# Kernel tuning notes

Hardware: AMD Instinct MI355X
Metric: run time of the kernel (lower is better)

Reference implementation:

```python
import jax, jax.numpy as jnp
import numpy as np

B, N, M, D, H = 2, 256, 64, 768, 12
HD = D // H  # head dim 64


def setup_inputs() -> dict:
    key = jax.random.key(0)
    ks = jax.random.split(key, 8)
    s = 0.02
    return {
        "x": jax.random.normal(ks[0], (B, N, D), jnp.float32),
        "sim_embeddings": jax.random.normal(ks[1], (B, N, M, D), jnp.float32),
        "Wq": jax.random.normal(ks[2], (D, D), jnp.float32) * s,
        "bq": jnp.zeros((D,), jnp.float32),
        "Wkv": jax.random.normal(ks[3], (D, 2 * D), jnp.float32) * s,
        "bkv": jnp.zeros((2 * D,), jnp.float32),
        "Wp": jax.random.normal(ks[4], (D, D), jnp.float32) * s,
        "bp": jnp.zeros((D,), jnp.float32),
    }


def reference(x, sim_embeddings, Wq, bq, Wkv, bkv, Wp, bp):
    # x: (B,N,D); sim_embeddings: (B,N,M,D)
    b, n, d = x.shape
    m = sim_embeddings.shape[2]
    scale = HD ** -0.5

    q = (x @ Wq + bq).reshape(b, n, H, HD).transpose(0, 2, 1, 3)  # (B,H,N,hd)

    kv_x = x @ Wkv + bkv                       # (B,N,2D)
    k_x, v_x = jnp.split(kv_x, 2, axis=-1)
    k_x = k_x.reshape(b, n, H, HD).transpose(0, 2, 1, 3)  # (B,H,N,hd) shared-global K
    v_x = v_x.reshape(b, n, H, HD).transpose(0, 2, 1, 3)

    kv_s = sim_embeddings @ Wkv + bkv          # (B,N,M,2D)
    k_s, v_s = jnp.split(kv_s, 2, axis=-1)
    k_s = k_s.reshape(b, n, m, H, HD).transpose(0, 3, 1, 2, 4)  # (B,H,N,M,hd) per-query local K
    v_s = v_s.reshape(b, n, m, H, HD).transpose(0, 3, 1, 2, 4)

    # scores over concatenated [global N keys | local M keys] without expanding K to (B,N,N+M,D)
    sg = jnp.einsum('bhnd,bhkd->bhnk', q, k_x) * scale   # (B,H,N,N)
    sl = jnp.einsum('bhnd,bhnmd->bhnm', q, k_s) * scale  # (B,H,N,M)
    attn = jax.nn.softmax(jnp.concatenate([sg, sl], axis=-1), axis=-1)
    ag, al = attn[..., :n], attn[..., n:]

    out = (jnp.einsum('bhnk,bhkd->bhnd', ag, v_x)
           + jnp.einsum('bhnm,bhnmd->bhnd', al, v_s))   # (B,H,N,hd)
    out = out.transpose(0, 2, 1, 3).reshape(b, n, d)
    return out @ Wp + bp
```

## Files before the change

### kernel.cpp

```cpp
#include <hip/hip_runtime.h>
#include <stdint.h>

#define DEV_INLINE __device__ __forceinline__

typedef __bf16 bf16x8 __attribute__((ext_vector_type(8)));
typedef float f32x4 __attribute__((ext_vector_type(4)));

typedef const __attribute__((address_space(1))) void* gas_ptr;
typedef __attribute__((address_space(3))) void* las_ptr;

DEV_INLINE unsigned short f2bf(float f) {
    union { __bf16 h; unsigned short u; } v;
    v.h = (__bf16)f;
    return v.u;
}

template <int N> DEV_INLINE void waitcnt_vm() {
    asm volatile("s_waitcnt vmcnt(%0)" :: "n"(N) : "memory");
}
DEV_INLINE void hard_barrier() {
    __builtin_amdgcn_sched_barrier(0);
    __builtin_amdgcn_s_barrier();
    __builtin_amdgcn_sched_barrier(0);
}

__global__ __launch_bounds__(256)
void prep_all_kernel(const float* __restrict__ x, unsigned short* __restrict__ xb,
                     const float* __restrict__ Wkv, unsigned short* __restrict__ wkvb,
                     const float* __restrict__ bq, const float* __restrict__ bkv,
                     float* __restrict__ bias1, float* __restrict__ zbuf,
                     const float* __restrict__ Wq, const float* __restrict__ Wp,
                     unsigned short* __restrict__ w1t, unsigned short* __restrict__ wpt,
                     const float* __restrict__ sim, unsigned short* __restrict__ simb) {
    __shared__ float tl[64][65];
    const int bid = blockIdx.x, t = threadIdx.x;
    if (bid >= 2124) {
        long i = (long)(bid - 2124) * 256 + t;
        const float4* sp = (const float4*)sim + i * 2;
        float4 a = sp[0], b = sp[1];
        union { bf16x8 v; unsigned short u[8]; } pk;
        pk.u[0] = f2bf(a.x); pk.u[1] = f2bf(a.y);
        pk.u[2] = f2bf(a.z); pk.u[3] = f2bf(a.w);
        pk.u[4] = f2bf(b.x); pk.u[5] = f2bf(b.y);
        pk.u[6] = f2bf(b.z); pk.u[7] = f2bf(b.w);
        ((bf16x8*)simb)[i] = pk.v;
        return;
    }
    if (bid < 1536) {
        const float* s; unsigned short* d; long i;
        if (bid < 384) { s = x;   d = xb;   i = (long)bid * 256 + t; }
        else           { s = Wkv; d = wkvb; i = (long)(bid - 384) * 256 + t; }
        float4 a = ((const float4*)s)[i];
        ushort4 o;
        o.x = f2bf(a.x); o.y = f2bf(a.y); o.z = f2bf(a.z); o.w = f2bf(a.w);
        ((ushort4*)d)[i] = o;
    } else if (bid < 1548) {
        int i = (bid - 1536) * 256 + t;
        if (i < 768) bias1[i] = bq[i];
        else if (i < 2304) bias1[i] = bkv[i - 768];
        else zbuf[i - 2304] = 0.f;
    } else {
        int tb = bid - 1548;
        int bx = tb % 48, by = tb / 48;
        const float* src; unsigned short* dst; int C;
        if (bx < 12)      { src = Wq;  dst = w1t;              C = 768; }
        else if (bx < 36) { src = Wkv; dst = w1t + 768L * 768; C = 1536; bx -= 12; }
        else              { src = Wp;  dst = wpt;              C = 768; bx -= 36; }
        int c0 = bx * 64, r0 = by * 64;
        int tx = t & 63, ty = t >> 6;
        #pragma unroll
        for (int i = 0; i < 64; i += 4)
            tl[ty + i][tx] = src[(long)(r0 + ty + i) * C + c0 + tx];
        __syncthreads();
        #pragma unroll
        for (int i = 0; i < 64; i += 4)
            dst[(long)(c0 + ty + i) * 768 + r0 + tx] = f2bf(tl[tx][ty + i]);
    }
}

template <int WM, int WN, int WAVES_M, bool G1E>
DEV_INLINE void gemm_body(const unsigned short* A, int lda,
                          const unsigned short* BT, int ldb,
                          const unsigned short* A2, int lda2,
                          const unsigned short* B2, int ldb2, int K1,
                          const float* bias, void* Cout, int ldc, int K,
                          const float* cin, int OUT, long obase, long tm, long tn,
                          unsigned short* As, unsigned short* Bs,
                          float* g1_qf, unsigned short* g1_qb,
                          unsigned short* g1_kxb, unsigned short* g1_vxT) {
    constexpr int TR = WAVES_M * WM * 16;
    constexpr int TC = (4 / WAVES_M) * WN * 16;
    constexpr int NL = TR / 32 + TC / 32;
    const int tid = threadIdx.x;
    const int w = tid >> 6, lane = tid & 63;
    const int lm = lane & 15, quad = lane >> 4;
    const int m_off = (w % WAVES_M) * WM * 16;
    const int n_off = (w / WAVES_M) * WN * 16;
    const int lrow8 = lane >> 3;
    const int lcol_sw = (((lane & 7) ^ lrow8) * 8);

    f32x4 acc[WM][WN];
    #pragma unroll
    for (int mi = 0; mi < WM; ++mi)
        #pragma unroll
        for (int ni = 0; ni < WN; ++ni) acc[mi][ni] = f32x4{0.f, 0.f, 0.f, 0.f};

    auto stage = [&](int k0, int pb) {
        const unsigned short* Ab; const unsigned short* Bb;
        int la, lb, kc;
        if (k0 < K1) { Ab = A;  Bb = BT; la = lda;  lb = ldb;  kc = k0; }
        else         { Ab = A2; Bb = B2; la = lda2; lb = ldb2; kc = k0 - K1; }
        unsigned short* Asb = As + pb * (TR * 64);
        unsigned short* Bsb = Bs + pb * (TC * 64);
        #pragma unroll
        for (int i = 0; i < TR / 32; ++i) {
            int rr = w * (TR / 4) + i * 8;
            const unsigned short* ga = Ab + (tm + rr + lrow8) * la + kc + lcol_sw;
            __builtin_amdgcn_global_load_lds((gas_ptr)ga, (las_ptr)(Asb + rr * 64), 16, 0, 0);
        }
        #pragma unroll
        for (int i = 0; i < TC / 32; ++i) {
            int rr = w * (TC / 4) + i * 8;
            const unsigned short* gb = Bb + (tn + rr + lrow8) * lb + kc + lcol_sw;
            __builtin_amdgcn_global_load_lds((gas_ptr)gb, (las_ptr)(Bsb + rr * 64), 16, 0, 0);
        }
    };

    stage(0, 0);
    const int nt = K >> 6;
    for (int t = 0; t < nt; ++t) {
        const int cur = t & 1;
        if (t + 1 < nt) {
            stage((t + 1) << 6, cur ^ 1);
            waitcnt_vm<NL>();
        } else {
            waitcnt_vm<0>();
        }
        hard_barrier();
        const unsigned short* Asb = As + cur * (TR * 64);
        const unsigned short* Bsb = Bs + cur * (TC * 64);
        #pragma unroll
        for (int kk = 0; kk < 2; ++kk) {
            bf16x8 af[WM], bfr[WN];
            #pragma unroll
            for (int mi = 0; mi < WM; ++mi) {
                int r = m_off + mi * 16 + lm;
                af[mi] = *(const bf16x8*)(Asb + r * 64 + (((kk * 4 + quad) ^ (r & 7)) * 8));
            }
            #pragma unroll
            for (int ni = 0; ni < WN; ++ni) {
                int r = n_off + ni * 16 + lm;
                bfr[ni] = *(const bf16x8*)(Bsb + r * 64 + (((kk * 4 + quad) ^ (r & 7)) * 8));
            }
            #pragma unroll
            for (int mi = 0; mi < WM; ++mi)
                #pragma unroll
                for (int ni = 0; ni < WN; ++ni)
                    acc[mi][ni] = __builtin_amdgcn_mfma_f32_16x16x32_bf16(
                        af[mi], bfr[ni], acc[mi][ni], 0, 0, 0);
        }
        hard_barrier();
    }

    #pragma unroll
    for (int mi = 0; mi < WM; ++mi) {
        #pragma unroll
        for (int ni = 0; ni < WN; ++ni) {
            long col = tn + n_off + ni * 16 + lm;
            float bv = bias[col];
            #pragma unroll
            for (int r = 0; r < 4; ++r) {
                long row = tm + m_off + mi * 16 + quad * 4 + r;
                float v = acc[mi][ni][r] + bv;
                if (G1E) {
                    if (col < 768) {
                        g1_qf[row * 768 + col] = v;
                        g1_qb[row * 768 + col] = f2bf(v);
                    } else if (col < 1536) {
                        g1_kxb[row * 768 + (col - 768)] = f2bf(v);
                    } else {
                        int j = (int)col - 1536, h = j >> 6, d = j & 63;
                        int bb = (int)row >> 8, nn = (int)row & 255;
                        g1_vxT[((long)(bb * 12 + h) * 64 + d) * 256 + nn] = f2bf(v);
                    }
                } else {
                    long idx = obase + row * ldc + col;
                    if (cin) v += cin[idx];
                    if (OUT == 0) ((float*)Cout)[idx] = v;
                    else ((unsigned short*)Cout)[idx] = f2bf(v);
                }
            }
        }
    }
}

template <int WM, int WN, int WAVES_M, bool G1E>
__global__ __launch_bounds__(256)
void gemm_bf16_kernel(const unsigned short* __restrict__ A, int lda,
                      const unsigned short* __restrict__ BT, int ldb,
                      const float* __restrict__ bias,
                      void* __restrict__ Cout, int ldc, int K,
                      const float* __restrict__ cin, int OUT,
                      long aZb, long aZh, long bZb, long bZh, long oZb, long oZh,
                      float* __restrict__ g1_qf, unsigned short* __restrict__ g1_qb,
                      unsigned short* __restrict__ g1_kxb,
                      unsigned short* __restrict__ g1_vxT) {
    constexpr int TR = WAVES_M * WM * 16;
    constexpr int TC = (4 / WAVES_M) * WN * 16;
    __shared__ unsigned short As[2 * TR * 64];
    __shared__ unsigned short Bs[2 * TC * 64];
    const int z = blockIdx.z, zb = z / 12, zh = z % 12;
    gemm_body<WM, WN, WAVES_M, G1E>(
        A + zb * aZb + zh * aZh, lda, BT + zb * bZb + zh * bZh, ldb,
        nullptr, 0, nullptr, 0, 1 << 30,
        bias, Cout, ldc, K, cin, OUT, zb * oZb + zh * oZh,
        (long)blockIdx.y * TR, (long)blockIdx.x * TC, As, Bs,
        g1_qf, g1_qb, g1_kxb, g1_vxT);
}

__global__ __launch_bounds__(256)
void gemm_qwsg_kernel(const unsigned short* __restrict__ qb,
                      const unsigned short* __restrict__ wkvb,
                      const unsigned short* __restrict__ kxb,
                      const float* __restrict__ zbuf,
                      unsigned short* __restrict__ qWb,
                      float* __restrict__ sgbuf) {
    __shared__ unsigned short As[2 * 64 * 64];
    __shared__ unsigned short Bs[2 * 64 * 64];
    int bid = blockIdx.x;
    if (bid < 1152) {
        int bx = bid % 12, by = (bid / 12) % 8, h = bid / 96;
        gemm_body<2, 2, 2, false>(
            qb + h * 64, 768, wkvb + h * 64, 1536,
            nullptr, 0, nullptr, 0, 1 << 30,
            zbuf, qWb, 768, 64, nullptr, 1, (long)h * 393216,
            (long)by * 64, (long)bx * 64, As, Bs,
            nullptr, nullptr, nullptr, nullptr);
    } else {
        int bid2 = bid - 1152;
        int bx = bid2 % 4, by = (bid2 / 4) % 4, z = bid2 / 16;
        int zb = z / 12, zh = z % 12;
        gemm_body<2, 2, 2, false>(
            qb + zb * 196608 + zh * 64, 768, kxb + zb * 196608 + zh * 64, 768,
            nullptr, 0, nullptr, 0, 1 << 30,
            zbuf, sgbuf, 256, 64, nullptr, 0,
            (long)zb * 786432 + (long)zh * 65536,
            (long)by * 64, (long)bx * 64, As, Bs,
            nullptr, nullptr, nullptr, nullptr);
    }
}

template <int WM, int WN, int WAVES_M>
__global__ __launch_bounds__(256)
void gemm_concat_kernel(const unsigned short* __restrict__ A, int lda, long aZb, long aZh,
                        const unsigned short* __restrict__ BT, int ldb, long bZb, long bZh,
                        const unsigned short* __restrict__ A2, int lda2, long a2Zb, long a2Zh,
                        const unsigned short* __restrict__ B2, int ldb2, long b2Zb, long b2Zh,
                        int K1, int K, const float* __restrict__ bias,
                        void* __restrict__ Cout, int ldc,
                        const float* __restrict__ cin, int OUT, long oZb, long oZh) {
    constexpr int TR = WAVES_M * WM * 16;
    constexpr int TC = (4 / WAVES_M) * WN * 16;
    __shared__ unsigned short As[2 * TR * 64];
    __shared__ unsigned short Bs[2 * TC * 64];
    const int z = blockIdx.z, zb = z / 12, zh = z % 12;
    gemm_body<WM, WN, WAVES_M, false>(
        A + zb * aZb + zh * aZh, lda, BT + zb * bZb + zh * bZh, ldb,
        A2 + zb * a2Zb + zh * a2Zh, lda2, B2 + zb * b2Zb + zh * b2Zh, ldb2, K1,
        bias, Cout, ldc, K, cin, OUT, zb * oZb + zh * oZh,
        (long)blockIdx.y * TR, (long)blockIdx.x * TC, As, Bs,
        nullptr, nullptr, nullptr, nullptr);
}

__global__ __launch_bounds__(256)
void slpart2_kernel(const unsigned short* __restrict__ simb,
                    const unsigned short* __restrict__ qWb,
                    float* __restrict__ sclp) {
    __shared__ unsigned short qw_s[16 * 784];
    __shared__ unsigned short ss[2][64 * 64];
    const int t = threadIdx.x;
    const int w = t >> 6, lane = t & 63;
    const int lm = lane & 15, quad = lane >> 4;
    const int lrow8 = lane >> 3;
    const int lcol_sw = ((lane & 7) ^ lrow8) * 8;
    const int n_ = blockIdx.x;
    const unsigned short* simn = simb + (long)n_ * 49152;

    auto stage = [&](int c, int pb) {
        unsigned short* dst = ss[pb];
        #pragma unroll
        for (int i = 0; i < 2; ++i) {
            int rr = w * 16 + i * 8;
            const unsigned short* ga = simn + (rr + lrow8) * 768 + c * 64 + lcol_sw;
            __builtin_amdgcn_global_load_lds((gas_ptr)ga, (las_ptr)(dst + rr * 64), 16, 0, 0);
        }
    };
    stage(0, 0);

    for (int idx = t; idx < 1152; idx += 256) {
        int h = idx / 96, c = idx - h * 96;
        *(bf16x8*)(qw_s + h * 784 + c * 8) =
            *(const bf16x8*)(qWb + ((long)h * 512 + n_) * 768 + c * 8);
    }
    __syncthreads();

    f32x4 acc = {};
    const int r = w * 16 + lm;
    for (int c = 0; c < 12; ++c) {
        const int cur = c & 1;
        if (c + 1 < 12) {
            stage(c + 1, cur ^ 1);
            waitcnt_vm<2>();
        } else {
            waitcnt_vm<0>();
        }
        hard_barrier();
        const unsigned short* buf = ss[cur];
        #pragma unroll
        for (int kk = 0; kk < 2; ++kk) {
            bf16x8 af = *(const bf16x8*)(buf + r * 64 + (((kk * 4 + quad) ^ (r & 7)) * 8));
            bf16x8 bfr = *(const bf16x8*)(qw_s + lm * 784 + c * 64 + kk * 32 + quad * 8);
            acc = __builtin_amdgcn_mfma_f32_16x16x32_bf16(af, bfr, acc, 0, 0, 0);
        }
        hard_barrier();
    }
    if (lm < 12) {
        float* dst = sclp + ((long)n_ * 12 + lm) * 64 + w * 16 + quad * 4;
        #pragma unroll
        for (int r2 = 0; r2 < 4; ++r2) dst[r2] = acc[r2];
    }
}

__global__ __launch_bounds__(256)
void attn2_kernel(const float* __restrict__ sim,
                  const float* __restrict__ qf,
                  const float* __restrict__ bkv,
                  const float* __restrict__ sclp,
                  const float* __restrict__ sgbuf,
                  unsigned short* __restrict__ agb,
                  float* __restrict__ outg0,
                  unsigned short* __restrict__ simbar) {
    __shared__ float slb_s[12];
    __shared__ float al_s[12][64];
    const int t = threadIdx.x;
    const int lane = t & 63, w = t >> 6;
    const int n_ = blockIdx.x, cg = blockIdx.y;
    const int b = n_ >> 8, n = n_ & 255;
    const float* simn = sim + (long)n_ * 49152;

    {
        float p0 = qf[(long)n_ * 768 + t] * bkv[t];
        float p1 = qf[(long)n_ * 768 + t + 256] * bkv[t + 256];
        float p2 = qf[(long)n_ * 768 + t + 512] * bkv[t + 512];
        #pragma unroll
        for (int off = 32; off > 0; off >>= 1) {
            p0 += __shfl_xor(p0, off);
            p1 += __shfl_xor(p1, off);
            p2 += __shfl_xor(p2, off);
        }
        if (lane == 0) { slb_s[w] = p0; slb_s[w + 4] = p1; slb_s[w + 8] = p2; }
    }
    __syncthreads();

    #pragma unroll
    for (int i = 0; i < 3; ++i) {
        const int h = w * 3 + i;
        const float* sgr = sgbuf + (long)(b * 12 + h) * 65536 + (long)n * 256;
        float v0 = sgr[lane] * 0.125f, v1 = sgr[lane + 64] * 0.125f,
              v2 = sgr[lane + 128] * 0.125f, v3 = sgr[lane + 192] * 0.125f;
        float v4 = (sclp[((long)n_ * 12 + h) * 64 + lane] + slb_s[h]) * 0.125f;
        float mx = fmaxf(fmaxf(fmaxf(v0, v1), fmaxf(v2, v3)), v4);
        #pragma unroll
        for (int off = 32; off > 0; off >>= 1) mx = fmaxf(mx, __shfl_xor(mx, off));
        float e0 = __expf(v0 - mx), e1 = __expf(v1 - mx), e2 = __expf(v2 - mx),
              e3 = __expf(v3 - mx), e4 = __expf(v4 - mx);
        float s = e0 + e1 + e2 + e3 + e4;
        #pragma unroll
        for (int off = 32; off > 0; off >>= 1) s += __shfl_xor(s, off);
        float inv = __frcp_rn(s);
        float al = e4 * inv;
        al_s[h][lane] = al;
        if (cg == 0) {
            unsigned short* agr = agb + (long)(b * 12 + h) * 65536 + (long)n * 256;
            agr[lane] = f2bf(e0 * inv); agr[lane + 64] = f2bf(e1 * inv);
            agr[lane + 128] = f2bf(e2 * inv); agr[lane + 192] = f2bf(e3 * inv);
            float am = al;
            #pragma unroll
            for (int off = 32; off > 0; off >>= 1) am += __shfl_xor(am, off);
            outg0[(long)n_ * 768 + h * 64 + lane] = am * bkv[768 + h * 64 + lane];
        }
    }
    __syncthreads();

    const int c = cg * 256 + t;
    float a[12];
    #pragma unroll
    for (int h = 0; h < 12; ++h) a[h] = 0.f;
    #pragma unroll 4
    for (int m = 0; m < 64; ++m) {
        float s = simn[(long)m * 768 + c];
        #pragma unroll
        for (int h = 0; h < 12; ++h) a[h] += al_s[h][m] * s;
    }
    #pragma unroll
    for (int h = 0; h < 12; ++h)
        simbar[((long)h * 512 + n_) * 768 + c] = f2bf(a[h]);
}


extern "C" void kernel_launch(void* const* d_in, const int* in_sizes, int n_in,
                              void* d_out, int out_size, void* d_ws, size_t ws_size,
                              hipStream_t stream) {
    const float* x   = (const float*)d_in[0];
    const float* sim = (const float*)d_in[1];
    const float* Wq  = (const float*)d_in[2];
    const float* bq  = (const float*)d_in[3];
    const float* Wkv = (const float*)d_in[4];
    const float* bkv = (const float*)d_in[5];
    const float* Wp  = (const float*)d_in[6];
    const float* bp  = (const float*)d_in[7];
    float* out = (float*)d_out;

    char* ws = (char*)d_ws;
    size_t off = 0;
    auto alloc = [&](size_t bytes) {
        char* p = ws + off;
        off += (bytes + 255) & ~(size_t)255;
        return p;
    };
    unsigned short* xb     = (unsigned short*)alloc(512UL * 768 * 2);
    unsigned short* w1t    = (unsigned short*)alloc(2304UL * 768 * 2);
    unsigned short* wkvb   = (unsigned short*)alloc(768UL * 1536 * 2);
    unsigned short* wpt    = (unsigned short*)alloc(768UL * 768 * 2);
    float*          qf     = (float*)alloc(512UL * 768 * 4);
    unsigned short* qb     = (unsigned short*)alloc(512UL * 768 * 2);
    unsigned short* kxb    = (unsigned short*)alloc(512UL * 768 * 2);
    unsigned short* vxT    = (unsigned short*)alloc(24UL * 64 * 256 * 2);
    unsigned short* qWb    = (unsigned short*)alloc(12UL * 512 * 768 * 2);
    unsigned short* simb   = (unsigned short*)alloc(512UL * 64 * 768 * 2);
    float*          sgbuf  = (float*)alloc(24UL * 65536 * 4);
    unsigned short* agb    = (unsigned short*)alloc(24UL * 65536 * 2);
    float*          outg0  = (float*)alloc(512UL * 768 * 4);
    float*          sclp   = (float*)alloc(512UL * 12 * 64 * 4);
    unsigned short* simbar = (unsigned short*)alloc(12UL * 512 * 768 * 2);
    unsigned short* attnb  = (unsigned short*)alloc(512UL * 768 * 2);
    float*          bias1  = (float*)alloc(2304UL * 4);
    float*          zbuf   = (float*)alloc(768UL * 4);

    prep_all_kernel<<<14412, 256, 0, stream>>>(
        x, xb, Wkv, wkvb, bq, bkv, bias1, zbuf, Wq, Wp, w1t, wpt, sim, simb);

    gemm_bf16_kernel<1, 2, 2, true><<<dim3(36, 16, 1), 256, 0, stream>>>(
        xb, 768, w1t, 768, bias1, nullptr, 768, 768, nullptr, 0,
        0, 0, 0, 0, 0, 0, qf, qb, kxb, vxT);

    gemm_qwsg_kernel<<<1536, 256, 0, stream>>>(qb, wkvb, kxb, zbuf, qWb, sgbuf);

    slpart2_kernel<<<512, 256, 0, stream>>>(simb, qWb, sclp);

    attn2_kernel<<<dim3(512, 3), 256, 0, stream>>>(
        sim, qf, bkv, sclp, sgbuf, agb, outg0, simbar);

    gemm_concat_kernel<1, 1, 2><<<dim3(2, 8, 24), 256, 0, stream>>>(
        simbar, 768, 196608, 393216,
        w1t + 1536L * 768, 768, 0, 49152,
        agb, 256, 786432, 65536,
        vxT, 256, 196608, 16384,
        768, 1024, zbuf, attnb, 768, outg0, 1, 196608, 64);

    gemm_bf16_kernel<1, 1, 2, false><<<dim3(24, 16, 1), 256, 0, stream>>>(
        attnb, 768, wpt, 768, bp, out, 768, 768, nullptr, 0,
        0, 0, 0, 0, 0, 0, nullptr, nullptr, nullptr, nullptr);
}
```

Baseline: 246.6 us.

## Fuse post-prep stages into one cooperative persistent kernel with grid syncs

Replaces the six kernel launches after prep with one cooperative kernel of 512 blocks that runs each stage in turn, separated by grid-wide syncs. The slpart and attn stages merge per row, so the local scores stay in LDS and the sclp buffer is gone. GEMM tile shapes change to a single 64x64 configuration, and the late GEMMs run on only 96 blocks. The aim is to remove launch gaps and a global round trip, at the cost of grid-sync overhead, less parallelism in the small GEMM phases, and each block doing three column groups serially in the attention phase.

New measurement: 706.1 us. 2.86x slower.

```diff
diff --git a/kernel.cpp b/kernel.cpp
--- a/kernel.cpp
+++ b/kernel.cpp
@@ -1,5 +1,8 @@
 #include <hip/hip_runtime.h>
+#include <hip/hip_cooperative_groups.h>
 #include <stdint.h>
+
+namespace cg = cooperative_groups;
 
 #define DEV_INLINE __device__ __forceinline__
 
@@ -194,217 +197,216 @@
     }
 }
 
-template <int WM, int WN, int WAVES_M, bool G1E>
-__global__ __launch_bounds__(256)
-void gemm_bf16_kernel(const unsigned short* __restrict__ A, int lda,
-                      const unsigned short* __restrict__ BT, int ldb,
-                      const float* __restrict__ bias,
-                      void* __restrict__ Cout, int ldc, int K,
-                      const float* __restrict__ cin, int OUT,
-                      long aZb, long aZh, long bZb, long bZh, long oZb, long oZh,
-                      float* __restrict__ g1_qf, unsigned short* __restrict__ g1_qb,
-                      unsigned short* __restrict__ g1_kxb,
-                      unsigned short* __restrict__ g1_vxT) {
-    constexpr int TR = WAVES_M * WM * 16;
-    constexpr int TC = (4 / WAVES_M) * WN * 16;
-    __shared__ unsigned short As[2 * TR * 64];
-    __shared__ unsigned short Bs[2 * TC * 64];
-    const int z = blockIdx.z, zb = z / 12, zh = z % 12;
-    gemm_body<WM, WN, WAVES_M, G1E>(
-        A + zb * aZb + zh * aZh, lda, BT + zb * bZb + zh * bZh, ldb,
-        nullptr, 0, nullptr, 0, 1 << 30,
-        bias, Cout, ldc, K, cin, OUT, zb * oZb + zh * oZh,
-        (long)blockIdx.y * TR, (long)blockIdx.x * TC, As, Bs,
-        g1_qf, g1_qb, g1_kxb, g1_vxT);
-}
-
-__global__ __launch_bounds__(256)
-void gemm_qwsg_kernel(const unsigned short* __restrict__ qb,
-                      const unsigned short* __restrict__ wkvb,
-                      const unsigned short* __restrict__ kxb,
-                      const float* __restrict__ zbuf,
-                      unsigned short* __restrict__ qWb,
-                      float* __restrict__ sgbuf) {
-    __shared__ unsigned short As[2 * 64 * 64];
-    __shared__ unsigned short Bs[2 * 64 * 64];
-    int bid = blockIdx.x;
-    if (bid < 1152) {
-        int bx = bid % 12, by = (bid / 12) % 8, h = bid / 96;
-        gemm_body<2, 2, 2, false>(
-            qb + h * 64, 768, wkvb + h * 64, 1536,
-            nullptr, 0, nullptr, 0, 1 << 30,
-            zbuf, qWb, 768, 64, nullptr, 1, (long)h * 393216,
-            (long)by * 64, (long)bx * 64, As, Bs,
-            nullptr, nullptr, nullptr, nullptr);
-    } else {
-        int bid2 = bid - 1152;
-        int bx = bid2 % 4, by = (bid2 / 4) % 4, z = bid2 / 16;
-        int zb = z / 12, zh = z % 12;
-        gemm_body<2, 2, 2, false>(
-            qb + zb * 196608 + zh * 64, 768, kxb + zb * 196608 + zh * 64, 768,
-            nullptr, 0, nullptr, 0, 1 << 30,
-            zbuf, sgbuf, 256, 64, nullptr, 0,
-            (long)zb * 786432 + (long)zh * 65536,
-            (long)by * 64, (long)bx * 64, As, Bs,
-            nullptr, nullptr, nullptr, nullptr);
-    }
-}
-
-template <int WM, int WN, int WAVES_M>
-__global__ __launch_bounds__(256)
-void gemm_concat_kernel(const unsigned short* __restrict__ A, int lda, long aZb, long aZh,
-                        const unsigned short* __restrict__ BT, int ldb, long bZb, long bZh,
-                        const unsigned short* __restrict__ A2, int lda2, long a2Zb, long a2Zh,
-                        const unsigned short* __restrict__ B2, int ldb2, long b2Zb, long b2Zh,
-                        int K1, int K, const float* __restrict__ bias,
-                        void* __restrict__ Cout, int ldc,
-                        const float* __restrict__ cin, int OUT, long oZb, long oZh) {
-    constexpr int TR = WAVES_M * WM * 16;
-    constexpr int TC = (4 / WAVES_M) * WN * 16;
-    __shared__ unsigned short As[2 * TR * 64];
-    __shared__ unsigned short Bs[2 * TC * 64];
-    const int z = blockIdx.z, zb = z / 12, zh = z % 12;
-    gemm_body<WM, WN, WAVES_M, false>(
-        A + zb * aZb + zh * aZh, lda, BT + zb * bZb + zh * bZh, ldb,
-        A2 + zb * a2Zb + zh * a2Zh, lda2, B2 + zb * b2Zb + zh * b2Zh, ldb2, K1,
-        bias, Cout, ldc, K, cin, OUT, zb * oZb + zh * oZh,
-        (long)blockIdx.y * TR, (long)blockIdx.x * TC, As, Bs,
-        nullptr, nullptr, nullptr, nullptr);
-}
-
-__global__ __launch_bounds__(256)
-void slpart2_kernel(const unsigned short* __restrict__ simb,
-                    const unsigned short* __restrict__ qWb,
-                    float* __restrict__ sclp) {
-    __shared__ unsigned short qw_s[16 * 784];
-    __shared__ unsigned short ss[2][64 * 64];
+struct MegaArgs {
+    const unsigned short* xb;
+    const unsigned short* w1t;
+    const unsigned short* wkvb;
+    const unsigned short* wpt;
+    const float* bias1;
+    const float* zbuf;
+    const float* bkv;
+    const float* bp;
+    float* qf;
+    unsigned short* qb;
+    unsigned short* kxb;
+    unsigned short* vxT;
+    unsigned short* qWb;
+    const unsigned short* simb;
+    const float* sim;
+    float* sgbuf;
+    unsigned short* agb;
+    float* outg0;
+    unsigned short* simbar;
+    unsigned short* attnb;
+    float* out;
+};
+
+union GSmem {
+    struct { unsigned short As[2 * 64 * 64]; unsigned short Bs[2 * 64 * 64]; } g;
+    struct { unsigned short qw[16 * 784]; unsigned short ss[2 * 64 * 64]; } sl;
+};
+
+__global__ __launch_bounds__(256, 2)
+void mega_kernel(MegaArgs a) {
+    __shared__ GSmem sm;
+    __shared__ float sclp_l[12][64];
+    __shared__ float al_l[12][64];
+    __shared__ float slb_l[12];
+    cg::grid_group grid = cg::this_grid();
+    const int bid = blockIdx.x;
     const int t = threadIdx.x;
     const int w = t >> 6, lane = t & 63;
     const int lm = lane & 15, quad = lane >> 4;
-    const int lrow8 = lane >> 3;
-    const int lcol_sw = ((lane & 7) ^ lrow8) * 8;
-    const int n_ = blockIdx.x;
-    const unsigned short* simn = simb + (long)n_ * 49152;
-
-    auto stage = [&](int c, int pb) {
-        unsigned short* dst = ss[pb];
-        #pragma unroll
-        for (int i = 0; i < 2; ++i) {
-            int rr = w * 16 + i * 8;
-            const unsigned short* ga = simn + (rr + lrow8) * 768 + c * 64 + lcol_sw;
-            __builtin_amdgcn_global_load_lds((gas_ptr)ga, (las_ptr)(dst + rr * 64), 16, 0, 0);
-        }
-    };
-    stage(0, 0);
-
-    for (int idx = t; idx < 1152; idx += 256) {
-        int h = idx / 96, c = idx - h * 96;
-        *(bf16x8*)(qw_s + h * 784 + c * 8) =
-            *(const bf16x8*)(qWb + ((long)h * 512 + n_) * 768 + c * 8);
-    }
-    __syncthreads();
-
-    f32x4 acc = {};
-    const int r = w * 16 + lm;
-    for (int c = 0; c < 12; ++c) {
-        const int cur = c & 1;
-        if (c + 1 < 12) {
-            stage(c + 1, cur ^ 1);
-            waitcnt_vm<2>();
+
+    if (bid < 288) {
+        int bx = bid % 36, by = bid / 36;
+        gemm_body<2, 2, 2, true>(
+            a.xb, 768, a.w1t, 768, nullptr, 0, nullptr, 0, 1 << 30,
+            a.bias1, nullptr, 768, 768, nullptr, 0, 0,
+            (long)by * 64, (long)bx * 64, sm.g.As, sm.g.Bs,
+            a.qf, a.qb, a.kxb, a.vxT);
+    }
+    __threadfence(); grid.sync();
+
+    for (int job = bid; job < 1536; job += 512) {
+        if (job < 1152) {
+            int bx = job % 12, by = (job / 12) % 8, h = job / 96;
+            gemm_body<2, 2, 2, false>(
+                a.qb + h * 64, 768, a.wkvb + h * 64, 1536,
+                nullptr, 0, nullptr, 0, 1 << 30,
+                a.zbuf, a.qWb, 768, 64, nullptr, 1, (long)h * 393216,
+                (long)by * 64, (long)bx * 64, sm.g.As, sm.g.Bs,
+                nullptr, nullptr, nullptr, nullptr);
         } else {
-            waitcnt_vm<0>();
-        }
-        hard_barrier();
-        const unsigned short* buf = ss[cur];
-        #pragma unroll
-        for (int kk = 0; kk < 2; ++kk) {
-            bf16x8 af = *(const bf16x8*)(buf + r * 64 + (((kk * 4 + quad) ^ (r & 7)) * 8));
-            bf16x8 bfr = *(const bf16x8*)(qw_s + lm * 784 + c * 64 + kk * 32 + quad * 8);
-            acc = __builtin_amdgcn_mfma_f32_16x16x32_bf16(af, bfr, acc, 0, 0, 0);
-        }
-        hard_barrier();
-    }
-    if (lm < 12) {
-        float* dst = sclp + ((long)n_ * 12 + lm) * 64 + w * 16 + quad * 4;
-        #pragma unroll
-        for (int r2 = 0; r2 < 4; ++r2) dst[r2] = acc[r2];
-    }
-}
-
-__global__ __launch_bounds__(256)
-void attn2_kernel(const float* __restrict__ sim,
-                  const float* __restrict__ qf,
-                  const float* __restrict__ bkv,
-                  const float* __restrict__ sclp,
-                  const float* __restrict__ sgbuf,
-                  unsigned short* __restrict__ agb,
-                  float* __restrict__ outg0,
-                  unsigned short* __restrict__ simbar) {
-    __shared__ float slb_s[12];
-    __shared__ float al_s[12][64];
-    const int t = threadIdx.x;
-    const int lane = t & 63, w = t >> 6;
-    const int n_ = blockIdx.x, cg = blockIdx.y;
-    const int b = n_ >> 8, n = n_ & 255;
-    const float* simn = sim + (long)n_ * 49152;
+            int j2 = job - 1152;
+            int bx = j2 % 4, by = (j2 / 4) % 4, z = j2 / 16;
+            int zb = z / 12, zh = z % 12;
+            gemm_body<2, 2, 2, false>(
+                a.qb + zb * 196608 + zh * 64, 768, a.kxb + zb * 196608 + zh * 64, 768,
+                nullptr, 0, nullptr, 0, 1 << 30,
+                a.zbuf, a.sgbuf, 256, 64, nullptr, 0,
+                (long)zb * 786432 + (long)zh * 65536,
+                (long)by * 64, (long)bx * 64, sm.g.As, sm.g.Bs,
+                nullptr, nullptr, nullptr, nullptr);
+        }
+    }
+    __threadfence(); grid.sync();
 
     {
-        float p0 = qf[(long)n_ * 768 + t] * bkv[t];
-        float p1 = qf[(long)n_ * 768 + t + 256] * bkv[t + 256];
-        float p2 = qf[(long)n_ * 768 + t + 512] * bkv[t + 512];
-        #pragma unroll
-        for (int off = 32; off > 0; off >>= 1) {
-            p0 += __shfl_xor(p0, off);
-            p1 += __shfl_xor(p1, off);
-            p2 += __shfl_xor(p2, off);
-        }
-        if (lane == 0) { slb_s[w] = p0; slb_s[w + 4] = p1; slb_s[w + 8] = p2; }
-    }
-    __syncthreads();
-
-    #pragma unroll
-    for (int i = 0; i < 3; ++i) {
-        const int h = w * 3 + i;
-        const float* sgr = sgbuf + (long)(b * 12 + h) * 65536 + (long)n * 256;
-        float v0 = sgr[lane] * 0.125f, v1 = sgr[lane + 64] * 0.125f,
-              v2 = sgr[lane + 128] * 0.125f, v3 = sgr[lane + 192] * 0.125f;
-        float v4 = (sclp[((long)n_ * 12 + h) * 64 + lane] + slb_s[h]) * 0.125f;
-        float mx = fmaxf(fmaxf(fmaxf(v0, v1), fmaxf(v2, v3)), v4);
-        #pragma unroll
-        for (int off = 32; off > 0; off >>= 1) mx = fmaxf(mx, __shfl_xor(mx, off));
-        float e0 = __expf(v0 - mx), e1 = __expf(v1 - mx), e2 = __expf(v2 - mx),
-              e3 = __expf(v3 - mx), e4 = __expf(v4 - mx);
-        float s = e0 + e1 + e2 + e3 + e4;
-        #pragma unroll
-        for (int off = 32; off > 0; off >>= 1) s += __shfl_xor(s, off);
-        float inv = __frcp_rn(s);
-        float al = e4 * inv;
-        al_s[h][lane] = al;
-        if (cg == 0) {
-            unsigned short* agr = agb + (long)(b * 12 + h) * 65536 + (long)n * 256;
+        const int n_ = bid;
+        const int b = n_ >> 8, n = n_ & 255;
+        const int lrow8 = lane >> 3;
+        const int lcol_sw = ((lane & 7) ^ lrow8) * 8;
+        const unsigned short* simn_b = a.simb + (long)n_ * 49152;
+        const float* simn = a.sim + (long)n_ * 49152;
+
+        auto stage = [&](int c, int pb) {
+            unsigned short* dst = sm.sl.ss + pb * 4096;
+            #pragma unroll
+            for (int i = 0; i < 2; ++i) {
+                int rr = w * 16 + i * 8;
+                const unsigned short* ga = simn_b + (rr + lrow8) * 768 + c * 64 + lcol_sw;
+                __builtin_amdgcn_global_load_lds((gas_ptr)ga, (las_ptr)(dst + rr * 64), 16, 0, 0);
+            }
+        };
+        stage(0, 0);
+
+        for (int idx = t; idx < 1152; idx += 256) {
+            int h = idx / 96, c = idx - h * 96;
+            *(bf16x8*)(sm.sl.qw + h * 784 + c * 8) =
+                *(const bf16x8*)(a.qWb + ((long)h * 512 + n_) * 768 + c * 8);
+        }
+        {
+            float p0 = a.qf[(long)n_ * 768 + t] * a.bkv[t];
+            float p1 = a.qf[(long)n_ * 768 + t + 256] * a.bkv[t + 256];
+            float p2 = a.qf[(long)n_ * 768 + t + 512] * a.bkv[t + 512];
+            #pragma unroll
+            for (int off = 32; off > 0; off >>= 1) {
+                p0 += __shfl_xor(p0, off);
+                p1 += __shfl_xor(p1, off);
+                p2 += __shfl_xor(p2, off);
+            }
+            if (lane == 0) { slb_l[w] = p0; slb_l[w + 4] = p1; slb_l[w + 8] = p2; }
+        }
+        __syncthreads();
+
+        f32x4 acc = {};
+        const int r = w * 16 + lm;
+        for (int c = 0; c < 12; ++c) {
+            const int cur = c & 1;
+            if (c + 1 < 12) {
+                stage(c + 1, cur ^ 1);
+                waitcnt_vm<2>();
+            } else {
+                waitcnt_vm<0>();
+            }
+            hard_barrier();
+            const unsigned short* buf = sm.sl.ss + cur * 4096;
+            #pragma unroll
+            for (int kk = 0; kk < 2; ++kk) {
+                bf16x8 af = *(const bf16x8*)(buf + r * 64 + (((kk * 4 + quad) ^ (r & 7)) * 8));
+                bf16x8 bfr = *(const bf16x8*)(sm.sl.qw + lm * 784 + c * 64 + kk * 32 + quad * 8);
+                acc = __builtin_amdgcn_mfma_f32_16x16x32_bf16(af, bfr, acc, 0, 0, 0);
+            }
+            hard_barrier();
+        }
+        if (lm < 12) {
+            #pragma unroll
+            for (int r2 = 0; r2 < 4; ++r2)
+                sclp_l[lm][w * 16 + quad * 4 + r2] = acc[r2];
+        }
+        __syncthreads();
+
+        #pragma unroll
+        for (int i = 0; i < 3; ++i) {
+            const int h = w * 3 + i;
+            const float* sgr = a.sgbuf + (long)(b * 12 + h) * 65536 + (long)n * 256;
+            float v0 = sgr[lane] * 0.125f, v1 = sgr[lane + 64] * 0.125f,
+                  v2 = sgr[lane + 128] * 0.125f, v3 = sgr[lane + 192] * 0.125f;
+            float v4 = (sclp_l[h][lane] + slb_l[h]) * 0.125f;
+            float mx = fmaxf(fmaxf(fmaxf(v0, v1), fmaxf(v2, v3)), v4);
+            #pragma unroll
+            for (int off = 32; off > 0; off >>= 1) mx = fmaxf(mx, __shfl_xor(mx, off));
+            float e0 = __expf(v0 - mx), e1 = __expf(v1 - mx), e2 = __expf(v2 - mx),
+                  e3 = __expf(v3 - mx), e4 = __expf(v4 - mx);
+            float s = e0 + e1 + e2 + e3 + e4;
+            #pragma unroll
+            for (int off = 32; off > 0; off >>= 1) s += __shfl_xor(s, off);
+            float inv = __frcp_rn(s);
+            unsigned short* agr = a.agb + (long)(b * 12 + h) * 65536 + (long)n * 256;
             agr[lane] = f2bf(e0 * inv); agr[lane + 64] = f2bf(e1 * inv);
             agr[lane + 128] = f2bf(e2 * inv); agr[lane + 192] = f2bf(e3 * inv);
+            float al = e4 * inv;
+            al_l[h][lane] = al;
             float am = al;
             #pragma unroll
             for (int off = 32; off > 0; off >>= 1) am += __shfl_xor(am, off);
-            outg0[(long)n_ * 768 + h * 64 + lane] = am * bkv[768 + h * 64 + lane];
-        }
-    }
-    __syncthreads();
-
-    const int c = cg * 256 + t;
-    float a[12];
-    #pragma unroll
-    for (int h = 0; h < 12; ++h) a[h] = 0.f;
-    #pragma unroll 4
-    for (int m = 0; m < 64; ++m) {
-        float s = simn[(long)m * 768 + c];
-        #pragma unroll
-        for (int h = 0; h < 12; ++h) a[h] += al_s[h][m] * s;
-    }
-    #pragma unroll
-    for (int h = 0; h < 12; ++h)
-        simbar[((long)h * 512 + n_) * 768 + c] = f2bf(a[h]);
+            a.outg0[(long)n_ * 768 + h * 64 + lane] = am * a.bkv[768 + h * 64 + lane];
+        }
+        __syncthreads();
+
+        #pragma unroll
+        for (int cg3 = 0; cg3 < 3; ++cg3) {
+            const int c = cg3 * 256 + t;
+            float av[12];
+            #pragma unroll
+            for (int h = 0; h < 12; ++h) av[h] = 0.f;
+            #pragma unroll 4
+            for (int m = 0; m < 64; ++m) {
+                float s = simn[(long)m * 768 + c];
+                #pragma unroll
+                for (int h = 0; h < 12; ++h) av[h] += al_l[h][m] * s;
+            }
+            #pragma unroll
+            for (int h = 0; h < 12; ++h)
+                a.simbar[((long)h * 512 + n_) * 768 + c] = f2bf(av[h]);
+        }
+    }
+    __threadfence(); grid.sync();
+
+    if (bid < 96) {
+        int by = bid % 4, z = bid / 4;
+        int zb = z / 12, zh = z % 12;
+        gemm_body<2, 2, 2, false>(
+            a.simbar + zb * 196608L + zh * 393216L, 768,
+            a.w1t + 1536L * 768 + zh * 49152L, 768,
+            a.agb + zb * 786432L + zh * 65536L, 256,
+            a.vxT + zb * 196608L + zh * 16384L, 256, 768,
+            a.zbuf, a.attnb, 768, 1024, a.outg0, 1,
+            (long)zb * 196608 + (long)zh * 64,
+            (long)by * 64, 0, sm.g.As, sm.g.Bs,
+            nullptr, nullptr, nullptr, nullptr);
+    }
+    __threadfence(); grid.sync();
+
+    if (bid < 96) {
+        int bx = bid % 12, by = bid / 12;
+        gemm_body<2, 2, 2, false>(
+            a.attnb, 768, a.wpt, 768, nullptr, 0, nullptr, 0, 1 << 30,
+            a.bp, a.out, 768, 768, nullptr, 0, 0,
+            (long)by * 64, (long)bx * 64, sm.g.As, sm.g.Bs,
+            nullptr, nullptr, nullptr, nullptr);
+    }
 }
 
 
@@ -441,7 +443,6 @@
     float*          sgbuf  = (float*)alloc(24UL * 65536 * 4);
     unsigned short* agb    = (unsigned short*)alloc(24UL * 65536 * 2);
     float*          outg0  = (float*)alloc(512UL * 768 * 4);
-    float*          sclp   = (float*)alloc(512UL * 12 * 64 * 4);
     unsigned short* simbar = (unsigned short*)alloc(12UL * 512 * 768 * 2);
     unsigned short* attnb  = (unsigned short*)alloc(512UL * 768 * 2);
     float*          bias1  = (float*)alloc(2304UL * 4);
@@ -450,25 +451,14 @@
     prep_all_kernel<<<14412, 256, 0, stream>>>(
         x, xb, Wkv, wkvb, bq, bkv, bias1, zbuf, Wq, Wp, w1t, wpt, sim, simb);
 
-    gemm_bf16_kernel<1, 2, 2, true><<<dim3(36, 16, 1), 256, 0, stream>>>(
-        xb, 768, w1t, 768, bias1, nullptr, 768, 768, nullptr, 0,
-        0, 0, 0, 0, 0, 0, qf, qb, kxb, vxT);
-
-    gemm_qwsg_kernel<<<1536, 256, 0, stream>>>(qb, wkvb, kxb, zbuf, qWb, sgbuf);
-
-    slpart2_kernel<<<512, 256, 0, stream>>>(simb, qWb, sclp);
-
-    attn2_kernel<<<dim3(512, 3), 256, 0, stream>>>(
-        sim, qf, bkv, sclp, sgbuf, agb, outg0, simbar);
-
-    gemm_concat_kernel<1, 1, 2><<<dim3(2, 8, 24), 256, 0, stream>>>(
-        simbar, 768, 196608, 393216,
-        w1t + 1536L * 768, 768, 0, 49152,
-        agb, 256, 786432, 65536,
-        vxT, 256, 196608, 16384,
-        768, 1024, zbuf, attnb, 768, outg0, 1, 196608, 64);
-
-    gemm_bf16_kernel<1, 1, 2, false><<<dim3(24, 16, 1), 256, 0, stream>>>(
-        attnb, 768, wpt, 768, bp, out, 768, 768, nullptr, 0,
-        0, 0, 0, 0, 0, 0, nullptr, nullptr, nullptr, nullptr);
-}
+    MegaArgs ma;
+    ma.xb = xb; ma.w1t = w1t; ma.wkvb = wkvb; ma.wpt = wpt;
+    ma.bias1 = bias1; ma.zbuf = zbuf; ma.bkv = bkv; ma.bp = bp;
+    ma.qf = qf; ma.qb = qb; ma.kxb = kxb; ma.vxT = vxT; ma.qWb = qWb;
+    ma.simb = simb; ma.sim = sim;
+    ma.sgbuf = sgbuf; ma.agb = agb; ma.outg0 = outg0;
+    ma.simbar = simbar; ma.attnb = attnb; ma.out = out;
+    void* kargs[] = { (void*)&ma };
+    hipLaunchCooperativeKernel((void*)mega_kernel, dim3(512), dim3(256),
+                               kargs, 0, stream);
+}
```

## Fuse sim bf16 conversion into split-K local score kernel

Applied to the files above, without the earlier changes.

Removes the separate fp32-to-bf16 pass over sim_embeddings from the prep kernel and instead converts each 64x64 tile on the fly inside the local-score kernel. The score kernel is split over the 12 K-chunks across a second grid dimension, writing per-chunk partials that the attention kernel sums. This avoids writing and re-reading a large bf16 copy of sim and increases parallelism, at the cost of a larger partial buffer and 12 extra loads per score in the softmax kernel.

After: 244.6 us. About the same (-0.8%).

```diff
diff --git a/kernel.cpp b/kernel.cpp
--- a/kernel.cpp
+++ b/kernel.cpp
@@ -30,22 +30,9 @@
                      const float* __restrict__ bq, const float* __restrict__ bkv,
                      float* __restrict__ bias1, float* __restrict__ zbuf,
                      const float* __restrict__ Wq, const float* __restrict__ Wp,
-                     unsigned short* __restrict__ w1t, unsigned short* __restrict__ wpt,
-                     const float* __restrict__ sim, unsigned short* __restrict__ simb) {
+                     unsigned short* __restrict__ w1t, unsigned short* __restrict__ wpt) {
     __shared__ float tl[64][65];
     const int bid = blockIdx.x, t = threadIdx.x;
-    if (bid >= 2124) {
-        long i = (long)(bid - 2124) * 256 + t;
-        const float4* sp = (const float4*)sim + i * 2;
-        float4 a = sp[0], b = sp[1];
-        union { bf16x8 v; unsigned short u[8]; } pk;
-        pk.u[0] = f2bf(a.x); pk.u[1] = f2bf(a.y);
-        pk.u[2] = f2bf(a.z); pk.u[3] = f2bf(a.w);
-        pk.u[4] = f2bf(b.x); pk.u[5] = f2bf(b.y);
-        pk.u[6] = f2bf(b.z); pk.u[7] = f2bf(b.w);
-        ((bf16x8*)simb)[i] = pk.v;
-        return;
-    }
     if (bid < 1536) {
         const float* s; unsigned short* d; long i;
         if (bid < 384) { s = x;   d = xb;   i = (long)bid * 256 + t; }
@@ -273,59 +260,51 @@
 }
 
 __global__ __launch_bounds__(256)
-void slpart2_kernel(const unsigned short* __restrict__ simb,
+void slpart3_kernel(const float* __restrict__ sim,
                     const unsigned short* __restrict__ qWb,
                     float* __restrict__ sclp) {
-    __shared__ unsigned short qw_s[16 * 784];
-    __shared__ unsigned short ss[2][64 * 64];
+    __shared__ unsigned short ss[64 * 64];
+    __shared__ unsigned short qwc[16 * 64];
     const int t = threadIdx.x;
-    const int w = t >> 6, lane = t & 63;
+    const int lane = t & 63, w = t >> 6;
     const int lm = lane & 15, quad = lane >> 4;
-    const int lrow8 = lane >> 3;
-    const int lcol_sw = ((lane & 7) ^ lrow8) * 8;
-    const int n_ = blockIdx.x;
-    const unsigned short* simn = simb + (long)n_ * 49152;
-
-    auto stage = [&](int c, int pb) {
-        unsigned short* dst = ss[pb];
-        #pragma unroll
-        for (int i = 0; i < 2; ++i) {
-            int rr = w * 16 + i * 8;
-            const unsigned short* ga = simn + (rr + lrow8) * 768 + c * 64 + lcol_sw;
-            __builtin_amdgcn_global_load_lds((gas_ptr)ga, (las_ptr)(dst + rr * 64), 16, 0, 0);
-        }
-    };
-    stage(0, 0);
-
-    for (int idx = t; idx < 1152; idx += 256) {
-        int h = idx / 96, c = idx - h * 96;
-        *(bf16x8*)(qw_s + h * 784 + c * 8) =
-            *(const bf16x8*)(qWb + ((long)h * 512 + n_) * 768 + c * 8);
+    const int n_ = blockIdx.x, c = blockIdx.y;
+    const float* simn = sim + (long)n_ * 49152 + c * 64;
+
+    {
+        int r = t >> 2, q = t & 3;
+        const float* gp = simn + (long)r * 768 + q * 16;
+        float4 a0 = *(const float4*)gp;
+        float4 a1 = *(const float4*)(gp + 4);
+        float4 a2 = *(const float4*)(gp + 8);
+        float4 a3 = *(const float4*)(gp + 12);
+        union { bf16x8 v; unsigned short u[8]; } p;
+        p.u[0] = f2bf(a0.x); p.u[1] = f2bf(a0.y); p.u[2] = f2bf(a0.z); p.u[3] = f2bf(a0.w);
+        p.u[4] = f2bf(a1.x); p.u[5] = f2bf(a1.y); p.u[6] = f2bf(a1.z); p.u[7] = f2bf(a1.w);
+        *(bf16x8*)(ss + r * 64 + (((q * 2) ^ (r & 7)) * 8)) = p.v;
+        p.u[0] = f2bf(a2.x); p.u[1] = f2bf(a2.y); p.u[2] = f2bf(a2.z); p.u[3] = f2bf(a2.w);
+        p.u[4] = f2bf(a3.x); p.u[5] = f2bf(a3.y); p.u[6] = f2bf(a3.z); p.u[7] = f2bf(a3.w);
+        *(bf16x8*)(ss + r * 64 + (((q * 2 + 1) ^ (r & 7)) * 8)) = p.v;
+    }
+    if (t < 96) {
+        int h = t >> 3, j = t & 7;
+        *(bf16x8*)(qwc + h * 64 + j * 8) =
+            *(const bf16x8*)(qWb + ((long)h * 512 + n_) * 768 + c * 64 + j * 8);
+    } else if (t < 128) {
+        *(bf16x8*)(qwc + 12 * 64 + (t - 96) * 8) = bf16x8{};
     }
     __syncthreads();
 
     f32x4 acc = {};
     const int r = w * 16 + lm;
-    for (int c = 0; c < 12; ++c) {
-        const int cur = c & 1;
-        if (c + 1 < 12) {
-            stage(c + 1, cur ^ 1);
-            waitcnt_vm<2>();
-        } else {
-            waitcnt_vm<0>();
-        }
-        hard_barrier();
-        const unsigned short* buf = ss[cur];
-        #pragma unroll
-        for (int kk = 0; kk < 2; ++kk) {
-            bf16x8 af = *(const bf16x8*)(buf + r * 64 + (((kk * 4 + quad) ^ (r & 7)) * 8));
-            bf16x8 bfr = *(const bf16x8*)(qw_s + lm * 784 + c * 64 + kk * 32 + quad * 8);
-            acc = __builtin_amdgcn_mfma_f32_16x16x32_bf16(af, bfr, acc, 0, 0, 0);
-        }
-        hard_barrier();
+    #pragma unroll
+    for (int kk = 0; kk < 2; ++kk) {
+        bf16x8 af = *(const bf16x8*)(ss + r * 64 + (((kk * 4 + quad) ^ (r & 7)) * 8));
+        bf16x8 bf_ = *(const bf16x8*)(qwc + lm * 64 + kk * 32 + quad * 8);
+        acc = __builtin_amdgcn_mfma_f32_16x16x32_bf16(af, bf_, acc, 0, 0, 0);
     }
     if (lm < 12) {
-        float* dst = sclp + ((long)n_ * 12 + lm) * 64 + w * 16 + quad * 4;
+        float* dst = sclp + (((long)c * 512 + n_) * 12 + lm) * 64 + w * 16 + quad * 4;
         #pragma unroll
         for (int r2 = 0; r2 < 4; ++r2) dst[r2] = acc[r2];
     }
@@ -368,7 +347,11 @@
         const float* sgr = sgbuf + (long)(b * 12 + h) * 65536 + (long)n * 256;
         float v0 = sgr[lane] * 0.125f, v1 = sgr[lane + 64] * 0.125f,
               v2 = sgr[lane + 128] * 0.125f, v3 = sgr[lane + 192] * 0.125f;
-        float v4 = (sclp[((long)n_ * 12 + h) * 64 + lane] + slb_s[h]) * 0.125f;
+        float sp = 0.f;
+        #pragma unroll
+        for (int cc = 0; cc < 12; ++cc)
+            sp += sclp[(((long)cc * 512 + n_) * 12 + h) * 64 + lane];
+        float v4 = (sp + slb_s[h]) * 0.125f;
         float mx = fmaxf(fmaxf(fmaxf(v0, v1), fmaxf(v2, v3)), v4);
         #pragma unroll
         for (int off = 32; off > 0; off >>= 1) mx = fmaxf(mx, __shfl_xor(mx, off));
@@ -437,18 +420,17 @@
     unsigned short* kxb    = (unsigned short*)alloc(512UL * 768 * 2);
     unsigned short* vxT    = (unsigned short*)alloc(24UL * 64 * 256 * 2);
     unsigned short* qWb    = (unsigned short*)alloc(12UL * 512 * 768 * 2);
-    unsigned short* simb   = (unsigned short*)alloc(512UL * 64 * 768 * 2);
     float*          sgbuf  = (float*)alloc(24UL * 65536 * 4);
     unsigned short* agb    = (unsigned short*)alloc(24UL * 65536 * 2);
     float*          outg0  = (float*)alloc(512UL * 768 * 4);
-    float*          sclp   = (float*)alloc(512UL * 12 * 64 * 4);
+    float*          sclp   = (float*)alloc(12UL * 512 * 12 * 64 * 4);
     unsigned short* simbar = (unsigned short*)alloc(12UL * 512 * 768 * 2);
     unsigned short* attnb  = (unsigned short*)alloc(512UL * 768 * 2);
     float*          bias1  = (float*)alloc(2304UL * 4);
     float*          zbuf   = (float*)alloc(768UL * 4);
 
-    prep_all_kernel<<<14412, 256, 0, stream>>>(
-        x, xb, Wkv, wkvb, bq, bkv, bias1, zbuf, Wq, Wp, w1t, wpt, sim, simb);
+    prep_all_kernel<<<2124, 256, 0, stream>>>(
+        x, xb, Wkv, wkvb, bq, bkv, bias1, zbuf, Wq, Wp, w1t, wpt);
 
     gemm_bf16_kernel<1, 2, 2, true><<<dim3(36, 16, 1), 256, 0, stream>>>(
         xb, 768, w1t, 768, bias1, nullptr, 768, 768, nullptr, 0,
@@ -456,7 +438,7 @@
 
     gemm_qwsg_kernel<<<1536, 256, 0, stream>>>(qb, wkvb, kxb, zbuf, qWb, sgbuf);
 
-    slpart2_kernel<<<512, 256, 0, stream>>>(simb, qWb, sclp);
+    slpart3_kernel<<<dim3(512, 12), 256, 0, stream>>>(sim, qWb, sclp);
 
     attn2_kernel<<<dim3(512, 3), 256, 0, stream>>>(
         sim, qf, bkv, sclp, sgbuf, agb, outg0, simbar);
```
